# Performance work log

Hardware: AMD Instinct MI355X
Metric: run time of the kernel (lower is better)

Reference implementation:

```python
import jax, jax.numpy as jnp
import numpy as np

D_MODEL = 1024
D_FF = 4096
NUM_EXPERTS = 8
TOP_K = 2
SEQ = 1024
BATCH = 2


def setup_inputs() -> dict:
    key = jax.random.key(0)
    ks = jax.random.split(key, 7)
    s = 0.02
    x = jax.random.normal(ks[0], (SEQ, BATCH, D_MODEL), dtype=jnp.float32)
    gate_w = jax.random.normal(ks[1], (D_MODEL, NUM_EXPERTS), dtype=jnp.float32) * s
    gate_b = jnp.zeros((NUM_EXPERTS,), dtype=jnp.float32)
    W1 = jax.random.normal(ks[2], (NUM_EXPERTS, D_MODEL, D_FF), dtype=jnp.float32) * s
    b1 = jnp.zeros((NUM_EXPERTS, D_FF), dtype=jnp.float32)
    W2 = jax.random.normal(ks[3], (NUM_EXPERTS, D_FF, D_MODEL), dtype=jnp.float32) * s
    b2 = jnp.zeros((NUM_EXPERTS, D_MODEL), dtype=jnp.float32)
    return {"x": x, "gate_w": gate_w, "gate_b": gate_b,
            "W1": W1, "b1": b1, "W2": W2, "b2": b2}


def reference(x, gate_w, gate_b, W1, b1, W2, b2):
    S, B, D = x.shape
    x_flat = x.reshape(-1, D)                       # [T, D], T = S*B
    scores = x_flat @ gate_w + gate_b               # [T, E]
    topk_vals, topk_idx = jax.lax.top_k(scores, TOP_K)   # [T, K]
    topk_probs = jax.nn.softmax(topk_vals, axis=-1)      # [T, K]
    # combine weight per (token, expert): sum of probs over slots routed to e
    one_hot = jax.nn.one_hot(topk_idx, NUM_EXPERTS, dtype=x.dtype)  # [T, K, E]
    combine = jnp.einsum('tk,tke->te', topk_probs, one_hot)         # [T, E]
    # dense per-expert FFN (tokens with combine weight 0 contribute nothing,
    # matching the masked gather/scatter in the torch loop)
    h = jax.nn.relu(jnp.einsum('td,edf->etf', x_flat, W1) + b1[:, None, :])  # [E, T, F]
    y = jnp.einsum('etf,efd->etd', h, W2) + b2[:, None, :]                    # [E, T, D]
    out = jnp.einsum('te,etd->td', combine, y)       # [T, D]
    return out.reshape(S, B, D)
```

## Files before the change

kernel.cpp:

```cpp
#include <hip/hip_runtime.h>
#include <stdint.h>

#define T_TOKENS 2048
#define DM 1024
#define DF 4096
#define NEXP 8
#define NSLOTS (T_TOKENS * 2)
#define HROWS (NSLOTS + 128)

typedef __bf16 bf16x8 __attribute__((ext_vector_type(8)));
typedef float f32x4 __attribute__((ext_vector_type(4)));

__device__ __forceinline__ ushort f2bf(float f) {
    union { float f; uint32_t u; } v; v.f = f;
    uint32_t r = v.u + 0x7FFFu + ((v.u >> 16) & 1u);
    return (ushort)(r >> 16);
}

__device__ __forceinline__ void gload16(const ushort* g, ushort* l) {
    __builtin_amdgcn_global_load_lds(
        (const __attribute__((address_space(1))) uint32_t*)g,
        (__attribute__((address_space(3))) uint32_t*)l,
        16, 0, 0);
}

__global__ void init_cnt(uint32_t* cnt) {
    if (threadIdx.x < NEXP) cnt[threadIdx.x] = 0;
}

__global__ __launch_bounds__(256) void gate_route(
    const float* __restrict__ x, const float* __restrict__ gw,
    const float* __restrict__ gb,
    uint32_t* __restrict__ route, uint32_t* __restrict__ cnt,
    float* __restrict__ prob, uint32_t* __restrict__ epk)
{
    const int w = threadIdx.x >> 6;
    const int lane = threadIdx.x & 63;
    const int t = blockIdx.x * 4 + w;
    float acc[NEXP];
#pragma unroll
    for (int e = 0; e < NEXP; ++e) acc[e] = 0.f;
    const float* xr = x + (size_t)t * DM;
#pragma unroll
    for (int j = 0; j < DM / 64; ++j) {
        const int d = j * 64 + lane;
        const float xv = xr[d];
        const float* g = gw + (size_t)d * NEXP;
#pragma unroll
        for (int e = 0; e < NEXP; ++e) acc[e] += xv * g[e];
    }
#pragma unroll
    for (int e = 0; e < NEXP; ++e) {
#pragma unroll
        for (int off = 32; off > 0; off >>= 1)
            acc[e] += __shfl_xor(acc[e], off);
        acc[e] += gb[e];
    }
    if (lane == 0) {
        int e0 = 0; float v0 = acc[0];
#pragma unroll
        for (int e = 1; e < NEXP; ++e) if (acc[e] > v0) { v0 = acc[e]; e0 = e; }
        int e1 = -1; float v1 = -1e30f;
#pragma unroll
        for (int e = 0; e < NEXP; ++e) if (e != e0 && acc[e] > v1) { v1 = acc[e]; e1 = e; }
        const float ex = expf(v1 - v0);
        const float inv = 1.f / (1.f + ex);
        prob[t * 2 + 0] = inv;
        prob[t * 2 + 1] = ex * inv;
        uint32_t pos = atomicAdd(&cnt[e0], 1u);
        route[e0 * T_TOKENS + pos] = (uint32_t)(t * 2);
        epk[t * 2] = ((uint32_t)e0 << 16) | pos;
        pos = atomicAdd(&cnt[e1], 1u);
        route[e1 * T_TOKENS + pos] = (uint32_t)(t * 2 + 1);
        epk[t * 2 + 1] = ((uint32_t)e1 << 16) | pos;
    }
}

__global__ void prefix_offs(const uint32_t* __restrict__ cnt,
                            uint32_t* __restrict__ offs)
{
    if (threadIdx.x == 0) {
        uint32_t a = 0;
#pragma unroll
        for (int e = 0; e < NEXP; ++e) { offs[e] = a; a += cnt[e]; }
        offs[NEXP] = a;
    }
}

__global__ __launch_bounds__(256) void convert_x(const float* __restrict__ x,
                                                 ushort* __restrict__ xb)
{
    const int i = (blockIdx.x * 256 + threadIdx.x) * 4;
    const float4 v = *reinterpret_cast<const float4*>(x + i);
    ushort4 o;
    o.x = f2bf(v.x); o.y = f2bf(v.y); o.z = f2bf(v.z); o.w = f2bf(v.w);
    *reinterpret_cast<ushort4*>(xb + i) = o;
}

template<int K, int N>
__global__ __launch_bounds__(256) void conv_transpose(const float* __restrict__ W,
                                                      ushort* __restrict__ Wb)
{
    const int e  = blockIdx.y;
    const int nt = blockIdx.x % (N / 64);
    const int kt = blockIdx.x / (N / 64);
    const int k0 = kt * 64, n0 = nt * 64;
    __shared__ ushort T[64][80];
    const int t = threadIdx.x;
    const int kr = t >> 4, nc = (t & 15) * 4;
    const float* src = W + ((size_t)e * K + k0 + kr) * N + n0 + nc;
#pragma unroll
    for (int i = 0; i < 4; ++i) {
        const float4 v = *reinterpret_cast<const float4*>(src + (size_t)i * 16 * N);
        T[nc + 0][kr + i * 16] = f2bf(v.x);
        T[nc + 1][kr + i * 16] = f2bf(v.y);
        T[nc + 2][kr + i * 16] = f2bf(v.z);
        T[nc + 3][kr + i * 16] = f2bf(v.w);
    }
    __syncthreads();
    const int r = t >> 2, c0 = t & 3;
    ushort* dst = Wb + ((size_t)e * N + n0 + r) * K + k0;
#pragma unroll
    for (int i = 0; i < 2; ++i) {
        const int c = c0 + i * 4;
        const uint4 v = *reinterpret_cast<const uint4*>(&T[r][c * 8]);
        *reinterpret_cast<uint4*>(dst + c * 8) = v;
    }
}

template<int KD, int ND, bool FIRST, int SPLIT, int NT>
__global__ __launch_bounds__(256, 4) void moe_gemm6(
    const ushort* __restrict__ Abuf,
    const ushort* __restrict__ Wb,
    const float* __restrict__ bias,
    const uint32_t* __restrict__ route,
    const uint32_t* __restrict__ cnt,
    const uint32_t* __restrict__ offs,
    const float* __restrict__ prob,
    ushort* __restrict__ hout,
    float* __restrict__ yout)
{
    const int bx = blockIdx.x;
    const int e  = bx / (16 * NT);
    const int mt = (bx / NT) & 15;
    const int nt = bx % NT;
    const uint32_t cntE = cnt[e];
    const int m0 = mt * 128;
    if ((uint32_t)m0 >= cntE) return;
    const uint32_t hb = offs[e];
    const int n0 = nt * 128;
    const int z  = (SPLIT > 1) ? (int)blockIdx.z : 0;
    const int kbeg = z * (KD / SPLIT);
    const int niter = (KD / SPLIT) / 32;

    __shared__ ushort As[2][128 * 32];
    __shared__ ushort Bs[2][128 * 32];
    __shared__ uint32_t s_route[128];
    __shared__ float s_p[128];

    const int tid = threadIdx.x;
    if (FIRST) {
        if (tid < 128) {
            const uint32_t idx = (uint32_t)(m0 + tid);
            const uint32_t s = (idx < cntE) ? route[e * T_TOKENS + idx] : 0u;
            s_route[tid] = s;
            s_p[tid] = prob[s];
        }
        __syncthreads();
    }

    const int w = tid >> 6, l = tid & 63;

    const ushort* asrc[2];
    const ushort* bsrc[2];
#pragma unroll
    for (int i = 0; i < 2; ++i) {
        const int chunk = (w * 2 + i) * 64 + l;
        const int row = chunk >> 2;
        const int c   = chunk & 3;
        const int cs  = c ^ ((row >> 1) & 3);
        size_t arow;
        if (FIRST) arow = (size_t)(s_route[row] >> 1);
        else       arow = (size_t)(hb + m0 + row);
        asrc[i] = Abuf + arow * KD + cs * 8 + kbeg;
        bsrc[i] = Wb + ((size_t)e * ND + n0 + row) * KD + cs * 8 + kbeg;
    }

    f32x4 acc[4][4];
#pragma unroll
    for (int i = 0; i < 4; ++i)
#pragma unroll
        for (int j = 0; j < 4; ++j) acc[i][j] = (f32x4){0.f, 0.f, 0.f, 0.f};

    const int q = l & 15, g = l >> 4;
    const int wm = w >> 1, wn = w & 1;

    int aoff[4], boff[4];
#pragma unroll
    for (int mi = 0; mi < 4; ++mi) {
        int row = wm * 64 + mi * 16 + q;
        aoff[mi] = row * 64 + (g ^ ((row >> 1) & 3)) * 16;
        row = wn * 64 + mi * 16 + q;
        boff[mi] = row * 64 + (g ^ ((row >> 1) & 3)) * 16;
    }

    ushort* const abase0 = &As[0][0];
    ushort* const bbase0 = &Bs[0][0];

#pragma unroll
    for (int i = 0; i < 2; ++i) gload16(asrc[i], abase0 + (w * 2 + i) * 512);
#pragma unroll
    for (int i = 0; i < 2; ++i) gload16(bsrc[i], bbase0 + (w * 2 + i) * 512);

    int cur = 0;
    for (int t = 0; t < niter; ++t) {
        if (t + 1 < niter) {
            ushort* ad = abase0 + (cur ^ 1) * (128 * 32) + (w * 2) * 512;
            ushort* bd = bbase0 + (cur ^ 1) * (128 * 32) + (w * 2) * 512;
            const int k1 = (t + 1) * 32;
#pragma unroll
            for (int i = 0; i < 2; ++i) gload16(asrc[i] + k1, ad + i * 512);
#pragma unroll
            for (int i = 0; i < 2; ++i) gload16(bsrc[i] + k1, bd + i * 512);
            asm volatile("s_waitcnt vmcnt(4)" ::: "memory");
        } else {
            asm volatile("s_waitcnt vmcnt(0)" ::: "memory");
        }
        __builtin_amdgcn_s_barrier();
        __builtin_amdgcn_sched_barrier(0);

        const char* Ab = (const char*)(abase0 + cur * (128 * 32));
        const char* Bb = (const char*)(bbase0 + cur * (128 * 32));
        bf16x8 af[4], bv[4];
#pragma unroll
        for (int mi = 0; mi < 4; ++mi)
            af[mi] = *reinterpret_cast<const bf16x8*>(Ab + aoff[mi]);
#pragma unroll
        for (int ni = 0; ni < 4; ++ni)
            bv[ni] = *reinterpret_cast<const bf16x8*>(Bb + boff[ni]);
        __builtin_amdgcn_s_setprio(1);
#pragma unroll
        for (int mi = 0; mi < 4; ++mi)
#pragma unroll
            for (int ni = 0; ni < 4; ++ni)
                acc[mi][ni] = __builtin_amdgcn_mfma_f32_16x16x32_bf16(
                    af[mi], bv[ni], acc[mi][ni], 0, 0, 0);
        __builtin_amdgcn_s_setprio(0);
        __builtin_amdgcn_s_barrier();
        cur ^= 1;
    }

#pragma unroll
    for (int mi = 0; mi < 4; ++mi) {
#pragma unroll
        for (int ni = 0; ni < 4; ++ni) {
            const int gcol = n0 + wn * 64 + ni * 16 + q;
#pragma unroll
            for (int j = 0; j < 4; ++j) {
                const int row = wm * 64 + mi * 16 + g * 4 + j;
                if ((uint32_t)(m0 + row) < cntE) {
                    const size_t grow = (size_t)(hb + m0 + row);
                    if (FIRST) {
                        float v = acc[mi][ni][j] + bias[e * ND + gcol];
                        v = fmaxf(v, 0.f) * s_p[row];
                        hout[grow * ND + gcol] = f2bf(v);
                    } else {
                        yout[((size_t)z * NSLOTS + grow) * ND + gcol] = acc[mi][ni][j];
                    }
                }
            }
        }
    }
}

__global__ __launch_bounds__(256) void combine5(
    const float* __restrict__ yc, const uint32_t* __restrict__ epk,
    const uint32_t* __restrict__ offs, const float* __restrict__ prob,
    const float* __restrict__ b2, float* __restrict__ out)
{
    const int gid = blockIdx.x * 256 + threadIdx.x;
    const int t = gid >> 8;
    const int dq = gid & 255;
    const uint32_t p0 = epk[2 * t], p1 = epk[2 * t + 1];
    const uint32_t e0 = p0 >> 16, e1 = p1 >> 16;
    const uint32_t r0 = offs[e0] + (p0 & 0xFFFFu);
    const uint32_t r1 = offs[e1] + (p1 & 0xFFFFu);
    const float w0 = prob[2 * t], w1 = prob[2 * t + 1];
    const float4 bb0 = reinterpret_cast<const float4*>(b2 + (size_t)e0 * DM)[dq];
    const float4 bb1 = reinterpret_cast<const float4*>(b2 + (size_t)e1 * DM)[dq];
    float4 o = { w0 * bb0.x + w1 * bb1.x, w0 * bb0.y + w1 * bb1.y,
                 w0 * bb0.z + w1 * bb1.z, w0 * bb0.w + w1 * bb1.w };
    const float4* Y = reinterpret_cast<const float4*>(yc);
#pragma unroll
    for (int zz = 0; zz < 4; ++zz) {
        const float4 a = Y[((size_t)zz * NSLOTS + r0) * 256 + dq];
        const float4 b = Y[((size_t)zz * NSLOTS + r1) * 256 + dq];
        o.x += a.x + b.x; o.y += a.y + b.y; o.z += a.z + b.z; o.w += a.w + b.w;
    }
    reinterpret_cast<float4*>(out)[gid] = o;
}

template<int KD, int ND, bool FIRST>
__global__ __launch_bounds__(256) void moe_gemm_v1(
    const ushort* __restrict__ Abuf, const float* __restrict__ W,
    const float* __restrict__ bias, const uint32_t* __restrict__ route,
    const uint32_t* __restrict__ cnt, const float* __restrict__ prob,
    ushort* __restrict__ hout, float* __restrict__ yout)
{
    const int e = blockIdx.x >> 4;
    const int mt = blockIdx.x & 15;
    const uint32_t cntE = cnt[e];
    const int m0 = mt * 128;
    if ((uint32_t)m0 >= cntE) return;
    const int n0 = blockIdx.y * 128;
    const int tid = threadIdx.x;
    __shared__ ushort Asm[128][40];
    __shared__ ushort Bsm[128][40];
    __shared__ uint32_t s_route[128];
    if (tid < 128) {
        const uint32_t idx = (uint32_t)(m0 + tid);
        s_route[tid] = (idx < cntE) ? route[e * T_TOKENS + idx] : 0xFFFFFFFFu;
    }
    __syncthreads();
    const int ar = tid >> 1, ah = tid & 1;
    const uint32_t s_a = s_route[ar];
    size_t arow = 0;
    if (s_a != 0xFFFFFFFFu) arow = FIRST ? (size_t)(s_a >> 1) : (size_t)s_a;
    const ushort* asrc = Abuf + arow * KD + ah * 16;
    const int c4 = tid & 31, kq = tid >> 5;
    const float* wbase = W + (size_t)e * KD * ND + (size_t)n0 + (size_t)c4 * 4;
    f32x4 acc[4][4];
#pragma unroll
    for (int i = 0; i < 4; ++i)
#pragma unroll
        for (int j = 0; j < 4; ++j) acc[i][j] = (f32x4){0.f, 0.f, 0.f, 0.f};
    const int lane = tid & 63, wv = tid >> 6;
    const int wm = wv >> 1, wn = wv & 1;
    const int q = lane & 15, g = lane >> 4;
    for (int k0 = 0; k0 < KD; k0 += 32) {
        {
            const uint4* src = reinterpret_cast<const uint4*>(asrc + k0);
            const uint4 v0 = src[0];
            const uint4 v1 = src[1];
            *reinterpret_cast<uint4*>(&Asm[ar][ah * 16]) = v0;
            *reinterpret_cast<uint4*>(&Asm[ar][ah * 16 + 8]) = v1;
        }
        {
            ushort vals[4][4];
#pragma unroll
            for (int r = 0; r < 4; ++r) {
                const float4 v = *reinterpret_cast<const float4*>(
                    wbase + (size_t)(k0 + kq * 4 + r) * ND);
                vals[r][0] = f2bf(v.x); vals[r][1] = f2bf(v.y);
                vals[r][2] = f2bf(v.z); vals[r][3] = f2bf(v.w);
            }
#pragma unroll
            for (int c = 0; c < 4; ++c) {
                const ushort4 o = { vals[0][c], vals[1][c], vals[2][c], vals[3][c] };
                *reinterpret_cast<ushort4*>(&Bsm[c4 * 4 + c][kq * 4]) = o;
            }
        }
        __syncthreads();
        bf16x8 af[4], bfr[4];
#pragma unroll
        for (int mi = 0; mi < 4; ++mi)
            af[mi] = *reinterpret_cast<const bf16x8*>(&Asm[wm * 64 + mi * 16 + q][g * 8]);
#pragma unroll
        for (int ni = 0; ni < 4; ++ni)
            bfr[ni] = *reinterpret_cast<const bf16x8*>(&Bsm[wn * 64 + ni * 16 + q][g * 8]);
#pragma unroll
        for (int mi = 0; mi < 4; ++mi)
#pragma unroll
            for (int ni = 0; ni < 4; ++ni)
                acc[mi][ni] = __builtin_amdgcn_mfma_f32_16x16x32_bf16(
                    af[mi], bfr[ni], acc[mi][ni], 0, 0, 0);
        __syncthreads();
    }
#pragma unroll
    for (int mi = 0; mi < 4; ++mi) {
#pragma unroll
        for (int ni = 0; ni < 4; ++ni) {
            const int gcol = n0 + wn * 64 + ni * 16 + q;
#pragma unroll
            for (int j = 0; j < 4; ++j) {
                const int row = wm * 64 + mi * 16 + g * 4 + j;
                if ((uint32_t)(m0 + row) < cntE) {
                    const uint32_t s = s_route[row];
                    float v = acc[mi][ni][j] + bias[e * ND + gcol];
                    if (FIRST) {
                        v = fmaxf(v, 0.f);
                        hout[(size_t)s * ND + gcol] = f2bf(v);
                    } else {
                        yout[(size_t)s * ND + gcol] = v * prob[s];
                    }
                }
            }
        }
    }
}

__global__ __launch_bounds__(256) void combine1(const float* __restrict__ yc,
                                                float* __restrict__ out)
{
    const int gid = blockIdx.x * 256 + threadIdx.x;
    const int t = gid >> 8;
    const int dq = gid & 255;
    const float4 va = reinterpret_cast<const float4*>(yc)[(size_t)(2 * t) * 256 + dq];
    const float4 vb = reinterpret_cast<const float4*>(yc)[(size_t)(2 * t + 1) * 256 + dq];
    const float4 o = { va.x + vb.x, va.y + vb.y, va.z + vb.z, va.w + vb.w };
    reinterpret_cast<float4*>(out)[gid] = o;
}

extern "C" void kernel_launch(void* const* d_in, const int* in_sizes, int n_in,
                              void* d_out, int out_size, void* d_ws, size_t ws_size,
                              hipStream_t stream)
{
    const float* x  = (const float*)d_in[0];
    const float* gw = (const float*)d_in[1];
    const float* gb = (const float*)d_in[2];
    const float* W1 = (const float*)d_in[3];
    const float* b1 = (const float*)d_in[4];
    const float* W2 = (const float*)d_in[5];
    const float* b2 = (const float*)d_in[6];
    float* out = (float*)d_out;
    char* ws = (char*)d_ws;

    const size_t OFF_XB    = 0;
    const size_t OFF_H     = 4194304;
    const size_t OFF_ROUTE = 38797312;
    const size_t OFF_CNT   = 38862848;
    const size_t OFF_OFFS  = 38862912;
    const size_t OFF_PROB  = 38862976;
    const size_t OFF_EPK   = 38879360;
    const size_t OFF_W1B   = 41943040;
    const size_t OFF_W2B   = 109051904;
    const size_t OFF_YC    = OFF_W1B;
    const size_t NEED      = 176160768ull;

    if (ws_size >= NEED) {
        ushort*   xb    = (ushort*)(ws + OFF_XB);
        ushort*   h     = (ushort*)(ws + OFF_H);
        float*    yc    = (float*)(ws + OFF_YC);
        uint32_t* route = (uint32_t*)(ws + OFF_ROUTE);
        uint32_t* cnt   = (uint32_t*)(ws + OFF_CNT);
        uint32_t* offs  = (uint32_t*)(ws + OFF_OFFS);
        float*    prob  = (float*)(ws + OFF_PROB);
        uint32_t* epk   = (uint32_t*)(ws + OFF_EPK);
        ushort*   w1b   = (ushort*)(ws + OFF_W1B);
        ushort*   w2b   = (ushort*)(ws + OFF_W2B);

        hipLaunchKernelGGL(init_cnt, dim3(1), dim3(64), 0, stream, cnt);
        hipLaunchKernelGGL(gate_route, dim3(T_TOKENS / 4), dim3(256), 0, stream,
                           x, gw, gb, route, cnt, prob, epk);
        hipLaunchKernelGGL(prefix_offs, dim3(1), dim3(64), 0, stream, cnt, offs);
        hipLaunchKernelGGL(convert_x, dim3(T_TOKENS * DM / 1024), dim3(256), 0, stream, x, xb);
        hipLaunchKernelGGL((conv_transpose<DM, DF>), dim3((DM / 64) * (DF / 64), NEXP),
                           dim3(256), 0, stream, W1, w1b);
        hipLaunchKernelGGL((moe_gemm6<DM, DF, true, 1, 32>),
                           dim3(NEXP * 16 * 32, 1, 1), dim3(256), 0, stream,
                           xb, w1b, b1, route, cnt, offs, prob, h, (float*)nullptr);
        hipLaunchKernelGGL((conv_transpose<DF, DM>), dim3((DF / 64) * (DM / 64), NEXP),
                           dim3(256), 0, stream, W2, w2b);
        hipLaunchKernelGGL((moe_gemm6<DF, DM, false, 4, 8>),
                           dim3(NEXP * 16 * 8, 1, 4), dim3(256), 0, stream,
                           h, w2b, (const float*)nullptr, route, cnt, offs,
                           (const float*)nullptr, (ushort*)nullptr, yc);
        hipLaunchKernelGGL(combine5, dim3(T_TOKENS * DM / 1024), dim3(256), 0, stream,
                           yc, epk, offs, prob, b2, out);
    } else {
        const size_t F_XB = 0, F_H = 4194304, F_YC = 37748736;
        const size_t F_ROUTE = 54525952, F_CNT = 54591488, F_PROB = 54591552;
        ushort*   xb    = (ushort*)(ws + F_XB);
        ushort*   h     = (ushort*)(ws + F_H);
        float*    yc    = (float*)(ws + F_YC);
        uint32_t* route = (uint32_t*)(ws + F_ROUTE);
        uint32_t* cnt   = (uint32_t*)(ws + F_CNT);
        float*    prob  = (float*)(ws + F_PROB);
        uint32_t* epk   = (uint32_t*)(ws + F_PROB + 16384);

        hipLaunchKernelGGL(init_cnt, dim3(1), dim3(64), 0, stream, cnt);
        hipLaunchKernelGGL(gate_route, dim3(T_TOKENS / 4), dim3(256), 0, stream,
                           x, gw, gb, route, cnt, prob, epk);
        hipLaunchKernelGGL(convert_x, dim3(T_TOKENS * DM / 1024), dim3(256), 0, stream, x, xb);
        hipLaunchKernelGGL((moe_gemm_v1<DM, DF, true>), dim3(NEXP * 16, DF / 128),
                           dim3(256), 0, stream, xb, W1, b1, route, cnt, prob,
                           h, (float*)nullptr);
        hipLaunchKernelGGL((moe_gemm_v1<DF, DM, false>), dim3(NEXP * 16, DM / 128),
                           dim3(256), 0, stream, h, W2, b2, route, cnt, prob,
                           (ushort*)nullptr, yc);
        hipLaunchKernelGGL(combine1, dim3(T_TOKENS * DM / 1024), dim3(256), 0, stream, yc, out);
    }
}
```

Before: 305.5 us.

## Enlarge MoE GEMM tiles to 256x256 with 512-thread blocks

Replaces the 128x128, 256-thread expert GEMM with a 256x256 tile computed by 512 threads (8 waves, each 128x64). Bigger tiles cut redundant global loads of weights and activations per FLOP. The LDS XOR swizzle is removed, the wait is moved to after the MFMA block so the next tile's loads overlap compute, and the bias load is hoisted out of the inner loop. Costs include possible LDS bank conflicts without the swizzle, more wasted rows when per-expert token counts don't fill a 256-row tile, fewer blocks to spread across CUs, and the padded H buffer shifting workspace offsets.

```diff
diff --git a/kernel.cpp b/kernel.cpp
--- a/kernel.cpp
+++ b/kernel.cpp
@@ -6,7 +6,7 @@
 #define DF 4096
 #define NEXP 8
 #define NSLOTS (T_TOKENS * 2)
-#define HROWS (NSLOTS + 128)
+#define HROWS (NSLOTS + 256)
 
 typedef __bf16 bf16x8 __attribute__((ext_vector_type(8)));
 typedef float f32x4 __attribute__((ext_vector_type(4)));
@@ -128,8 +128,8 @@
     }
 }
 
-template<int KD, int ND, bool FIRST, int SPLIT, int NT>
-__global__ __launch_bounds__(256, 4) void moe_gemm6(
+template<int KD, int ND, bool FIRST, int SPLIT, int NMT, int NT>
+__global__ __launch_bounds__(512, 2) void moe_gemm7(
     const ushort* __restrict__ Abuf,
     const ushort* __restrict__ Wb,
     const float* __restrict__ bias,
@@ -141,26 +141,26 @@
     float* __restrict__ yout)
 {
     const int bx = blockIdx.x;
-    const int e  = bx / (16 * NT);
-    const int mt = (bx / NT) & 15;
+    const int e  = bx / (NMT * NT);
+    const int mt = (bx / NT) % NMT;
     const int nt = bx % NT;
     const uint32_t cntE = cnt[e];
-    const int m0 = mt * 128;
+    const int m0 = mt * 256;
     if ((uint32_t)m0 >= cntE) return;
     const uint32_t hb = offs[e];
-    const int n0 = nt * 128;
+    const int n0 = nt * 256;
     const int z  = (SPLIT > 1) ? (int)blockIdx.z : 0;
     const int kbeg = z * (KD / SPLIT);
     const int niter = (KD / SPLIT) / 32;
 
-    __shared__ ushort As[2][128 * 32];
-    __shared__ ushort Bs[2][128 * 32];
-    __shared__ uint32_t s_route[128];
-    __shared__ float s_p[128];
+    __shared__ ushort As[2][256 * 32];
+    __shared__ ushort Bs[2][256 * 32];
+    __shared__ uint32_t s_route[256];
+    __shared__ float s_p[256];
 
     const int tid = threadIdx.x;
     if (FIRST) {
-        if (tid < 128) {
+        if (tid < 256) {
             const uint32_t idx = (uint32_t)(m0 + tid);
             const uint32_t s = (idx < cntE) ? route[e * T_TOKENS + idx] : 0u;
             s_route[tid] = s;
@@ -178,31 +178,29 @@
         const int chunk = (w * 2 + i) * 64 + l;
         const int row = chunk >> 2;
         const int c   = chunk & 3;
-        const int cs  = c ^ ((row >> 1) & 3);
         size_t arow;
         if (FIRST) arow = (size_t)(s_route[row] >> 1);
         else       arow = (size_t)(hb + m0 + row);
-        asrc[i] = Abuf + arow * KD + cs * 8 + kbeg;
-        bsrc[i] = Wb + ((size_t)e * ND + n0 + row) * KD + cs * 8 + kbeg;
-    }
-
-    f32x4 acc[4][4];
-#pragma unroll
-    for (int i = 0; i < 4; ++i)
+        asrc[i] = Abuf + arow * KD + c * 8 + kbeg;
+        bsrc[i] = Wb + ((size_t)e * ND + n0 + row) * KD + c * 8 + kbeg;
+    }
+
+    f32x4 acc[8][4];
+#pragma unroll
+    for (int i = 0; i < 8; ++i)
 #pragma unroll
         for (int j = 0; j < 4; ++j) acc[i][j] = (f32x4){0.f, 0.f, 0.f, 0.f};
 
     const int q = l & 15, g = l >> 4;
-    const int wm = w >> 1, wn = w & 1;
-
-    int aoff[4], boff[4];
-#pragma unroll
-    for (int mi = 0; mi < 4; ++mi) {
-        int row = wm * 64 + mi * 16 + q;
-        aoff[mi] = row * 64 + (g ^ ((row >> 1) & 3)) * 16;
-        row = wn * 64 + mi * 16 + q;
-        boff[mi] = row * 64 + (g ^ ((row >> 1) & 3)) * 16;
-    }
+    const int wm = w >> 2, wn = w & 3;
+
+    int aoff[8], boff[4];
+#pragma unroll
+    for (int mi = 0; mi < 8; ++mi)
+        aoff[mi] = (wm * 128 + mi * 16 + q) * 64 + g * 16;
+#pragma unroll
+    for (int ni = 0; ni < 4; ++ni)
+        boff[ni] = (wn * 64 + ni * 16 + q) * 64 + g * 16;
 
     ushort* const abase0 = &As[0][0];
     ushort* const bbase0 = &Bs[0][0];
@@ -211,57 +209,57 @@
     for (int i = 0; i < 2; ++i) gload16(asrc[i], abase0 + (w * 2 + i) * 512);
 #pragma unroll
     for (int i = 0; i < 2; ++i) gload16(bsrc[i], bbase0 + (w * 2 + i) * 512);
+    asm volatile("s_waitcnt vmcnt(0)" ::: "memory");
+    __builtin_amdgcn_s_barrier();
 
     int cur = 0;
+#pragma unroll 1
     for (int t = 0; t < niter; ++t) {
         if (t + 1 < niter) {
-            ushort* ad = abase0 + (cur ^ 1) * (128 * 32) + (w * 2) * 512;
-            ushort* bd = bbase0 + (cur ^ 1) * (128 * 32) + (w * 2) * 512;
+            ushort* ad = abase0 + (cur ^ 1) * (256 * 32) + (w * 2) * 512;
+            ushort* bd = bbase0 + (cur ^ 1) * (256 * 32) + (w * 2) * 512;
             const int k1 = (t + 1) * 32;
 #pragma unroll
             for (int i = 0; i < 2; ++i) gload16(asrc[i] + k1, ad + i * 512);
 #pragma unroll
             for (int i = 0; i < 2; ++i) gload16(bsrc[i] + k1, bd + i * 512);
-            asm volatile("s_waitcnt vmcnt(4)" ::: "memory");
-        } else {
-            asm volatile("s_waitcnt vmcnt(0)" ::: "memory");
-        }
-        __builtin_amdgcn_s_barrier();
-        __builtin_amdgcn_sched_barrier(0);
-
-        const char* Ab = (const char*)(abase0 + cur * (128 * 32));
-        const char* Bb = (const char*)(bbase0 + cur * (128 * 32));
-        bf16x8 af[4], bv[4];
-#pragma unroll
-        for (int mi = 0; mi < 4; ++mi)
-            af[mi] = *reinterpret_cast<const bf16x8*>(Ab + aoff[mi]);
+        }
+        const char* Ab = (const char*)(abase0 + cur * (256 * 32));
+        const char* Bb = (const char*)(bbase0 + cur * (256 * 32));
+        bf16x8 af[8], bv[4];
 #pragma unroll
         for (int ni = 0; ni < 4; ++ni)
             bv[ni] = *reinterpret_cast<const bf16x8*>(Bb + boff[ni]);
+#pragma unroll
+        for (int mi = 0; mi < 8; ++mi)
+            af[mi] = *reinterpret_cast<const bf16x8*>(Ab + aoff[mi]);
         __builtin_amdgcn_s_setprio(1);
 #pragma unroll
-        for (int mi = 0; mi < 4; ++mi)
+        for (int mi = 0; mi < 8; ++mi)
 #pragma unroll
             for (int ni = 0; ni < 4; ++ni)
                 acc[mi][ni] = __builtin_amdgcn_mfma_f32_16x16x32_bf16(
                     af[mi], bv[ni], acc[mi][ni], 0, 0, 0);
         __builtin_amdgcn_s_setprio(0);
+        asm volatile("s_waitcnt vmcnt(0)" ::: "memory");
         __builtin_amdgcn_s_barrier();
         cur ^= 1;
     }
 
 #pragma unroll
-    for (int mi = 0; mi < 4; ++mi) {
+    for (int mi = 0; mi < 8; ++mi) {
 #pragma unroll
         for (int ni = 0; ni < 4; ++ni) {
             const int gcol = n0 + wn * 64 + ni * 16 + q;
+            float bvx = 0.f;
+            if (FIRST) bvx = bias[e * ND + gcol];
 #pragma unroll
             for (int j = 0; j < 4; ++j) {
-                const int row = wm * 64 + mi * 16 + g * 4 + j;
+                const int row = wm * 128 + mi * 16 + g * 4 + j;
                 if ((uint32_t)(m0 + row) < cntE) {
                     const size_t grow = (size_t)(hb + m0 + row);
                     if (FIRST) {
-                        float v = acc[mi][ni][j] + bias[e * ND + gcol];
+                        float v = acc[mi][ni][j] + bvx;
                         v = fmaxf(v, 0.f) * s_p[row];
                         hout[grow * ND + gcol] = f2bf(v);
                     } else {
@@ -427,11 +425,11 @@
 
     const size_t OFF_XB    = 0;
     const size_t OFF_H     = 4194304;
-    const size_t OFF_ROUTE = 38797312;
-    const size_t OFF_CNT   = 38862848;
-    const size_t OFF_OFFS  = 38862912;
-    const size_t OFF_PROB  = 38862976;
-    const size_t OFF_EPK   = 38879360;
+    const size_t OFF_ROUTE = 39845888;
+    const size_t OFF_CNT   = 39911424;
+    const size_t OFF_OFFS  = 39911488;
+    const size_t OFF_PROB  = 39911552;
+    const size_t OFF_EPK   = 39927936;
     const size_t OFF_W1B   = 41943040;
     const size_t OFF_W2B   = 109051904;
     const size_t OFF_YC    = OFF_W1B;
@@ -456,13 +454,13 @@
         hipLaunchKernelGGL(convert_x, dim3(T_TOKENS * DM / 1024), dim3(256), 0, stream, x, xb);
         hipLaunchKernelGGL((conv_transpose<DM, DF>), dim3((DM / 64) * (DF / 64), NEXP),
                            dim3(256), 0, stream, W1, w1b);
-        hipLaunchKernelGGL((moe_gemm6<DM, DF, true, 1, 32>),
-                           dim3(NEXP * 16 * 32, 1, 1), dim3(256), 0, stream,
+        hipLaunchKernelGGL((moe_gemm7<DM, DF, true, 1, 8, 16>),
+                           dim3(NEXP * 8 * 16, 1, 1), dim3(512), 0, stream,
                            xb, w1b, b1, route, cnt, offs, prob, h, (float*)nullptr);
         hipLaunchKernelGGL((conv_transpose<DF, DM>), dim3((DF / 64) * (DM / 64), NEXP),
                            dim3(256), 0, stream, W2, w2b);
-        hipLaunchKernelGGL((moe_gemm6<DF, DM, false, 4, 8>),
-                           dim3(NEXP * 16 * 8, 1, 4), dim3(256), 0, stream,
+        hipLaunchKernelGGL((moe_gemm7<DF, DM, false, 4, 8, 4>),
+                           dim3(NEXP * 8 * 4, 1, 4), dim3(512), 0, stream,
                            h, w2b, (const float*)nullptr, route, cnt, offs,
                            (const float*)nullptr, (ushort*)nullptr, yc);
         hipLaunchKernelGGL(combine5, dim3(T_TOKENS * DM / 1024), dim3(256), 0, stream,
```

Measured after the change: 425.6 us. 39.3% more time.
